# Kernel optimization log

Measured on AMD Instinct MI355X. Metric: run time of the kernel, lower is better.

The kernel has to match this reference:

```python
import jax, jax.numpy as jnp
import numpy as np
import math

B, R, C = 4, 512, 512
E, H, D, M, F = 256, 16, 16, 16, 512  # embed, heads, qkv_dim, ms_hidden, ff_hidden
EPS = 1e-5


def setup_inputs() -> dict:
    key = jax.random.key(0)
    ks = jax.random.split(key, 20)
    s = lambda fan_in: 1.0 / math.sqrt(fan_in)
    u = lambda k, shape, lim: jax.random.uniform(k, shape, jnp.float32, -lim, lim)
    mix1_init = (1 / 2) ** 0.5
    mix2_init = (1 / 16) ** 0.5
    return {
        "row_emb": jax.random.normal(ks[0], (B, R, E), jnp.float32),
        "col_emb": jax.random.normal(ks[1], (B, C, E), jnp.float32),
        "cost_mat": jax.random.uniform(ks[2], (B, R, C), jnp.float32),
        "Wq": u(ks[3], (E, H * D), s(E)),
        "Wk": u(ks[4], (E, H * D), s(E)),
        "Wv": u(ks[5], (E, H * D), s(E)),
        "mix1_w": u(ks[6], (H, 2, M), mix1_init),
        "mix1_b": u(ks[7], (H, M), mix1_init),
        "mix2_w": u(ks[8], (H, M, 1), mix2_init),
        "mix2_b": u(ks[9], (H, 1), mix2_init),
        "Wc": u(ks[10], (H * D, E), s(H * D)),
        "bc": u(ks[11], (E,), s(H * D)),
        "W1": u(ks[12], (E, F), s(E)),
        "b1": u(ks[13], (F,), s(E)),
        "W2": u(ks[14], (F, E), s(F)),
        "b2": u(ks[15], (E,), s(F)),
        "g1": jnp.ones((E,), jnp.float32),
        "be1": jnp.zeros((E,), jnp.float32),
        "g2": jnp.ones((E,), jnp.float32),
        "be2": jnp.zeros((E,), jnp.float32),
    }


def _instance_norm(x, gamma, beta):
    # InstanceNorm1d on x permuted to (B, E, L): normalize over seq dim per (b, channel)
    mean = jnp.mean(x, axis=1, keepdims=True)          # [B,1,E]
    var = jnp.mean((x - mean) ** 2, axis=1, keepdims=True)
    return (x - mean) * jax.lax.rsqrt(var + EPS) * gamma + beta


def reference(row_emb, col_emb, cost_mat, Wq, Wk, Wv, mix1_w, mix1_b, mix2_w,
              mix2_b, Wc, bc, W1, b1, W2, b2, g1, be1, g2, be2):
    # QKV projections, split heads: [B,L,H*D] -> [B,H,L,D]
    q = (row_emb @ Wq).reshape(B, R, H, D).transpose(0, 2, 1, 3)
    k = (col_emb @ Wk).reshape(B, C, H, D).transpose(0, 2, 1, 3)
    v = (col_emb @ Wv).reshape(B, C, H, D).transpose(0, 2, 1, 3)

    dot = jnp.einsum('bhrd,bhcd->bhrc', q, k) / math.sqrt(D)
    cost = jnp.broadcast_to(cost_mat[:, None, :, :], (B, H, R, C))
    two = jnp.stack((dot, cost), axis=-1)               # [B,H,R,C,2]

    # per-head 2 -> M -> 1 mixing MLP over scores
    ms1 = jnp.einsum('bhrcs,hsm->bhrcm', two, mix1_w) + mix1_b[None, :, None, None, :]
    ms1 = jax.nn.relu(ms1)
    mixed = jnp.einsum('bhrcm,hm->bhrc', ms1, mix2_w[:, :, 0]) + mix2_b[:, 0][None, :, None, None]

    weights = jax.nn.softmax(mixed, axis=-1)            # [B,H,R,C]
    out = jnp.einsum('bhrc,bhcd->bhrd', weights, v)
    out_concat = out.transpose(0, 2, 1, 3).reshape(B, R, H * D)

    mh = out_concat @ Wc + bc                           # multi_head_combine

    # TransformerFFN with instance norm
    x = _instance_norm(row_emb + mh, g1, be1)
    ffn = jax.nn.relu(x @ W1 + b1) @ W2 + b2
    return _instance_norm(x + ffn, g2, be2)
```

## Files before the change

### kernel.cpp

```cpp
#include <hip/hip_runtime.h>
#include <hip/hip_bf16.h>

typedef __hip_bfloat16 bf16;
typedef __hip_bfloat162 bf162;
typedef _Float16 f16;
typedef __attribute__((ext_vector_type(2))) _Float16 h2;
typedef __attribute__((ext_vector_type(8))) short short8;
typedef __attribute__((ext_vector_type(4))) float f32x4;

#define B_ 4
#define R_ 512
#define C_ 512
#define E_ 256
#define H_ 16
#define D_ 16

__device__ __forceinline__ float b2f(bf16 x) { return __bfloat162float(x); }
__device__ __forceinline__ void stout(bf16* p, float v) { *p = __float2bfloat16(v); }
__device__ __forceinline__ void stout(f16* p, float v) { *p = (f16)v; }

__device__ __forceinline__ float fdot2(h2 a, h2 b, float c) {
#if __has_builtin(__builtin_amdgcn_fdot2)
    return __builtin_amdgcn_fdot2(a, b, c, false);
#else
    return (float)a.x * (float)b.x + (float)a.y * (float)b.y + c;
#endif
}

__global__ __launch_bounds__(256) void transpose_cvt_kernel(
    const float* __restrict__ Wq, const float* __restrict__ Wk, const float* __restrict__ Wv,
    const float* __restrict__ Wc, const float* __restrict__ W1, const float* __restrict__ W2,
    bf16* __restrict__ WqT, bf16* __restrict__ WkT, bf16* __restrict__ WvT,
    bf16* __restrict__ WcT, bf16* __restrict__ W1T, bf16* __restrict__ W2T,
    float* __restrict__ statsZ)
{
    __shared__ bf16 tile[32][33];
    const int wsel = blockIdx.y;
    const int tx = blockIdx.x;
    if (wsel == 0 && tx >= 64) {
        const int idx = (tx - 64) * 256 + threadIdx.x;
        if (idx < 4096) statsZ[idx] = 0.f;
        return;
    }
    const float* src; bf16* dst; int K, N;
    switch (wsel) {
        case 0: src = Wq; dst = WqT; K = 256; N = 256; break;
        case 1: src = Wk; dst = WkT; K = 256; N = 256; break;
        case 2: src = Wv; dst = WvT; K = 256; N = 256; break;
        case 3: src = Wc; dst = WcT; K = 256; N = 256; break;
        case 4: src = W1; dst = W1T; K = 256; N = 512; break;
        default: src = W2; dst = W2T; K = 512; N = 256; break;
    }
    const int ntiles = (K >> 5) * (N >> 5);
    if (tx >= ntiles) return;
    const int ncnt = N >> 5;
    const int tk = tx / ncnt, tn = tx % ncnt;
    const int c = threadIdx.x & 31, r = threadIdx.x >> 5;
#pragma unroll
    for (int i = 0; i < 4; i++)
        tile[r + i * 8][c] = __float2bfloat16(src[(size_t)(tk * 32 + r + i * 8) * N + tn * 32 + c]);
    __syncthreads();
#pragma unroll
    for (int i = 0; i < 4; i++)
        dst[(size_t)(tn * 32 + r + i * 8) * K + tk * 32 + c] = tile[c][r + i * 8];
}

template <int AMODE, typename OT, int BM, int BN, bool BIAS, int RES, bool RELU, bool STATS>
__device__ __forceinline__ void mfma_gemm_body(
    const void* __restrict__ Ap, const bf16* __restrict__ plA,
    const bf16* __restrict__ BT, const float* __restrict__ bias,
    const void* __restrict__ Res,
    const float* __restrict__ normS, const float* __restrict__ normG, const float* __restrict__ normB,
    float* __restrict__ statsOut, OT* __restrict__ Cout,
    int M, int N, int K, int bx, int by)
{
    constexpr int MT = BM / 32, NT = BN / 32;
    constexpr int AEL = BM * 64 / 256, BEL = BN * 64 / 256;
    __shared__ __align__(16) bf16 As[BM * 80];
    __shared__ __align__(16) bf16 Bs[BN * 80];
    const int tid = threadIdx.x;
    const int wid = tid >> 6, lane = tid & 63;
    const int wm = wid >> 1, wn = wid & 1;
    const int fr = lane & 15, quad = lane >> 4;
    const int m0 = by * BM, n0 = bx * BN;
    const int arow = (AEL == 16) ? (tid >> 2) : (tid >> 3);
    const int akg  = (AEL == 16) ? ((tid & 3) << 4) : ((tid & 7) << 3);
    const int brow = (BEL == 16) ? (tid >> 2) : (tid >> 3);
    const int bkg  = (BEL == 16) ? ((tid & 3) << 4) : ((tid & 7) << 3);

    f32x4 acc[MT][NT];
#pragma unroll
    for (int mt = 0; mt < MT; mt++)
#pragma unroll
        for (int nt = 0; nt < NT; nt++) acc[mt][nt] = (f32x4){0.f, 0.f, 0.f, 0.f};

    for (int k0 = 0; k0 < K; k0 += 64) {
        if constexpr (AMODE == 0) {
            const short8* gp = (const short8*)((const bf16*)Ap + (size_t)(m0 + arow) * K + k0 + akg);
#pragma unroll
            for (int t8 = 0; t8 < AEL / 8; t8++) *(short8*)(&As[arow * 80 + akg + 8 * t8]) = gp[t8];
        } else if constexpr (AMODE == 1) {
            const float4* gp = (const float4*)((const float*)Ap + (size_t)(m0 + arow) * K + k0 + akg);
#pragma unroll
            for (int j = 0; j < AEL / 4; j++) {
                const float4 f = gp[j];
                *(bf162*)(&As[arow * 80 + akg + j * 4])     = __float22bfloat162_rn(make_float2(f.x, f.y));
                *(bf162*)(&As[arow * 80 + akg + j * 4 + 2]) = __float22bfloat162_rn(make_float2(f.z, f.w));
            }
        } else if constexpr (AMODE == 2) {
            const int bb = (m0 + arow) >> 9;
            const bf16* ap = (const bf16*)Ap + (size_t)(m0 + arow) * K + k0 + akg;
            bf16 tmp[AEL];
#pragma unroll
            for (int t8 = 0; t8 < AEL / 8; t8++) *(short8*)(tmp + 8 * t8) = ((const short8*)ap)[t8];
#pragma unroll
            for (int j = 0; j < AEL; j++) {
                const int e = k0 + akg + j;
                const float s = normS[bb * 256 + e], sq = normS[1024 + bb * 256 + e];
                const float mn = s * (1.f / 512.f);
                float var = sq * (1.f / 512.f) - mn * mn; var = fmaxf(var, 0.f);
                As[arow * 80 + akg + j] = __float2bfloat16(
                    (b2f(tmp[j]) - mn) * rsqrtf(var + 1e-5f) * normG[e] + normB[e]);
            }
        } else {
            const int row = m0 + arow;
            const int bb = row >> 9, rr2 = row & 511;
            const int e0 = k0 + akg;
            const int hh = e0 >> 4, d0 = e0 & 15;
            const int idx = ((bb * 16 + hh) << 9) + rr2;
            const float l0 = b2f(plA[idx]), l1 = b2f(plA[32768 + idx]);
            const float l2 = b2f(plA[65536 + idx]), l3 = b2f(plA[98304 + idx]);
            const float inv = 1.f / (l0 + l1 + l2 + l3);
            const bf16* pob = (const bf16*)Ap;
            float a8[8] = {};
#pragma unroll
            for (int c = 0; c < 4; c++) {
                const float wgt = ((c == 0) ? l0 : (c == 1) ? l1 : (c == 2) ? l2 : l3) * inv;
                const bf162* pp = (const bf162*)(pob + (size_t)(c * 32768 + idx) * 16 + d0);
#pragma unroll
                for (int j = 0; j < 4; j++) {
                    const float2 f = __bfloat1622float2(pp[j]);
                    a8[2 * j]     = fmaf(wgt, f.x, a8[2 * j]);
                    a8[2 * j + 1] = fmaf(wgt, f.y, a8[2 * j + 1]);
                }
            }
#pragma unroll
            for (int j = 0; j < 8; j++)
                As[arow * 80 + akg + j] = __float2bfloat16(a8[j]);
        }
        {
            const short8* gp = (const short8*)(BT + (size_t)(n0 + brow) * K + k0 + bkg);
#pragma unroll
            for (int t8 = 0; t8 < BEL / 8; t8++) *(short8*)(&Bs[brow * 80 + bkg + 8 * t8]) = gp[t8];
        }
        __syncthreads();

        short8 af[MT][2], bfr[NT][2];
#pragma unroll
        for (int mt = 0; mt < MT; mt++) {
            const int ar = wm * (BM / 2) + mt * 16 + fr;
#pragma unroll
            for (int kh = 0; kh < 2; kh++)
                af[mt][kh] = *(const short8*)(&As[ar * 80 + quad * 8 + kh * 32]);
        }
#pragma unroll
        for (int nt = 0; nt < NT; nt++) {
            const int br = wn * (BN / 2) + nt * 16 + fr;
#pragma unroll
            for (int kh = 0; kh < 2; kh++)
                bfr[nt][kh] = *(const short8*)(&Bs[br * 80 + quad * 8 + kh * 32]);
        }
#pragma unroll
        for (int kh = 0; kh < 2; kh++)
#pragma unroll
            for (int mt = 0; mt < MT; mt++)
#pragma unroll
                for (int nt = 0; nt < NT; nt++)
                    acc[mt][nt] = __builtin_amdgcn_mfma_f32_16x16x32_bf16(
                        af[mt][kh], bfr[nt][kh], acc[mt][nt], 0, 0, 0);
        __syncthreads();
    }

    float vsum[NT], vss[NT];
#pragma unroll
    for (int nt = 0; nt < NT; nt++) { vsum[nt] = 0.f; vss[nt] = 0.f; }
#pragma unroll
    for (int mt = 0; mt < MT; mt++) {
#pragma unroll
        for (int nt = 0; nt < NT; nt++) {
#pragma unroll
            for (int i = 0; i < 4; i++) {
                const int row = m0 + wm * (BM / 2) + mt * 16 + quad * 4 + i;
                const int col = n0 + wn * (BN / 2) + nt * 16 + fr;
                float v = acc[mt][nt][i];
                if (BIAS) v += bias[col];
                if constexpr (RES == 1) v += ((const float*)Res)[(size_t)row * N + col];
                if constexpr (RES == 3) {
                    const int bb = row >> 9;
                    const float yv = b2f(((const bf16*)Res)[(size_t)row * N + col]);
                    const float s = normS[bb * 256 + col], sq = normS[1024 + bb * 256 + col];
                    const float mn = s * (1.f / 512.f);
                    float var = sq * (1.f / 512.f) - mn * mn; var = fmaxf(var, 0.f);
                    v += (yv - mn) * rsqrtf(var + 1e-5f) * normG[col] + normB[col];
                }
                if (RELU) v = fmaxf(v, 0.f);
                stout(&Cout[(size_t)row * N + col], v);
                if (STATS) { vsum[nt] += v; vss[nt] += v * v; }
            }
        }
    }
    if constexpr (STATS) {
        float* sred = (float*)As;
#pragma unroll
        for (int nt = 0; nt < NT; nt++) {
            float a = vsum[nt]; a += __shfl_xor(a, 16, 64); a += __shfl_xor(a, 32, 64);
            float c = vss[nt];  c += __shfl_xor(c, 16, 64); c += __shfl_xor(c, 32, 64);
            if (quad == 0) {
                const int cl = wn * (BN / 2) + nt * 16 + fr;
                sred[wm * (2 * BN) + cl * 2 + 0] = a;
                sred[wm * (2 * BN) + cl * 2 + 1] = c;
            }
        }
        __syncthreads();
        if (tid < 2 * BN) {
            const int cl = tid >> 1, w = tid & 1;
            const float tot = sred[cl * 2 + w] + sred[2 * BN + cl * 2 + w];
            atomicAdd(&statsOut[w * 1024 + (m0 >> 9) * 256 + n0 + cl], tot);
        }
    }
}

template <int AMODE, typename OT, int BM, int BN, bool BIAS, int RES, bool RELU, bool STATS>
__global__ __launch_bounds__(256) void mfma_gemm_kernel(
    const void* __restrict__ Ap, const bf16* __restrict__ plA,
    const bf16* __restrict__ BT, const float* __restrict__ bias,
    const void* __restrict__ Res,
    const float* __restrict__ normS, const float* __restrict__ normG, const float* __restrict__ normB,
    float* __restrict__ statsOut, OT* __restrict__ Cout, int M, int N, int K)
{
    mfma_gemm_body<AMODE, OT, BM, BN, BIAS, RES, RELU, STATS>(
        Ap, plA, BT, bias, Res, normS, normG, normB, statsOut, Cout,
        M, N, K, blockIdx.x, blockIdx.y);
}

__global__ __launch_bounds__(256) void qkv_kernel(
    const float* __restrict__ rowE, const float* __restrict__ colE,
    const bf16* __restrict__ WqT, const bf16* __restrict__ WkT, const bf16* __restrict__ WvT,
    f16* __restrict__ qo, f16* __restrict__ ko, f16* __restrict__ vo)
{
    const int z = blockIdx.z;
    const float* A = (z == 0) ? rowE : colE;
    const bf16* BT = (z == 0) ? WqT : (z == 1) ? WkT : WvT;
    f16* O = (z == 0) ? qo : (z == 1) ? ko : vo;
    mfma_gemm_body<1, f16, 32, 64, false, 0, false, false>(
        A, nullptr, BT, nullptr, nullptr, nullptr, nullptr, nullptr, nullptr, O,
        2048, 256, 256, blockIdx.x, blockIdx.y);
}

__global__ __launch_bounds__(256) void attn_kernel(
    const f16* __restrict__ q, const f16* __restrict__ k, const f16* __restrict__ v,
    const float* __restrict__ cost, const float* __restrict__ m1w, const float* __restrict__ m1b,
    const float* __restrict__ m2w, const float* __restrict__ m2b,
    bf16* __restrict__ po, bf16* __restrict__ plb)
{
    __shared__ __align__(16) char slds[17408];
    f16* kbuf = (f16*)slds;
    float* vbuf = (float*)(slds + 4096);
    float* sm = (float*)slds;

    const int rt = blockIdx.x >> 2, cs = blockIdx.x & 3;
    const int h = blockIdx.y, b = blockIdx.z;
    const int tid = threadIdx.x, wid = tid >> 6, lane = tid & 63;

    {
        const size_t base = ((size_t)b * C_) * 256 + h * 16 + (size_t)cs * 128 * 256;
        const int lc = tid >> 1, dp = (tid & 1) * 8;
        const size_t g = base + (size_t)lc * 256 + dp;
        *(short8*)(&kbuf[lc * 16 + dp]) = *(const short8*)(k + g);
        const short8 vraw = *(const short8*)(v + g);
        const h2* rh = (const h2*)&vraw;
        *(float4*)(&vbuf[lc * 16 + dp]) = make_float4(
            (float)rh[0].x, (float)rh[0].y, (float)rh[1].x, (float)rh[1].y);
        *(float4*)(&vbuf[lc * 16 + dp + 4]) = make_float4(
            (float)rh[2].x, (float)rh[2].y, (float)rh[3].x, (float)rh[3].y);
    }

    h2 w1a2[8], w1b2[8], b1h[8], w2p[8];
#pragma unroll
    for (int i = 0; i < 8; i++) {
        h2 t;
        t.x = (f16)m1w[h * 32 + 2 * i];      t.y = (f16)m1w[h * 32 + 2 * i + 1];      w1a2[i] = t;
        t.x = (f16)m1w[h * 32 + 16 + 2 * i]; t.y = (f16)m1w[h * 32 + 17 + 2 * i];     w1b2[i] = t;
        t.x = (f16)m1b[h * 16 + 2 * i];      t.y = (f16)m1b[h * 16 + 2 * i + 1];      b1h[i] = t;
        t.x = (f16)m2w[h * 16 + 2 * i];      t.y = (f16)m2w[h * 16 + 2 * i + 1];      w2p[i] = t;
    }
    const float b2v = m2b[h];
    const h2 zero2 = (h2)(f16)0;

    const int r = rt * 64 + lane;
    short8 qraw[2];
    {
        const short8* qp = (const short8*)(q + (size_t)(b * R_ + r) * 256 + h * 16);
        qraw[0] = qp[0]; qraw[1] = qp[1];
    }
    const h2* qh = (const h2*)qraw;

    __syncthreads();

    const float* crow = cost + (size_t)(b * R_ + r) * C_ + cs * 128 + wid * 32;
    float lrun = 0.f;
    float o[16] = {};

    for (int cc = 0; cc < 32; cc += 4) {
        const float4 cst4 = *(const float4*)(crow + cc);
#pragma unroll
        for (int u = 0; u < 4; u++) {
            const int lc = wid * 32 + cc + u;
            const h2* kr = (const h2*)(&kbuf[lc * 16]);
            float d = 0.f;
#pragma unroll
            for (int i = 0; i < 8; i++) d = fdot2(qh[i], kr[i], d);
            const float dot = d * 0.25f;
            const float cst = (u == 0) ? cst4.x : (u == 1) ? cst4.y : (u == 2) ? cst4.z : cst4.w;
            const f16 doth = (f16)dot, csth = (f16)cst;
            h2 dot2; dot2.x = doth; dot2.y = doth;
            h2 cst2; cst2.x = csth; cst2.y = csth;
            float acc = b2v;
#pragma unroll
            for (int i = 0; i < 8; i++) {
                h2 t = dot2 * w1a2[i] + b1h[i];
                t = cst2 * w1b2[i] + t;
                t = __builtin_elementwise_max(t, zero2);
                acc = fdot2(t, w2p[i], acc);
            }
            const float p = __expf(acc);
            lrun += p;
            const float4* vr = (const float4*)(&vbuf[lc * 16]);
            const float4 v0 = vr[0], v1 = vr[1], v2 = vr[2], v3 = vr[3];
            o[0]  = fmaf(p, v0.x, o[0]);  o[1]  = fmaf(p, v0.y, o[1]);
            o[2]  = fmaf(p, v0.z, o[2]);  o[3]  = fmaf(p, v0.w, o[3]);
            o[4]  = fmaf(p, v1.x, o[4]);  o[5]  = fmaf(p, v1.y, o[5]);
            o[6]  = fmaf(p, v1.z, o[6]);  o[7]  = fmaf(p, v1.w, o[7]);
            o[8]  = fmaf(p, v2.x, o[8]);  o[9]  = fmaf(p, v2.y, o[9]);
            o[10] = fmaf(p, v2.z, o[10]); o[11] = fmaf(p, v2.w, o[11]);
            o[12] = fmaf(p, v3.x, o[12]); o[13] = fmaf(p, v3.y, o[13]);
            o[14] = fmaf(p, v3.z, o[14]); o[15] = fmaf(p, v3.w, o[15]);
        }
    }

    __syncthreads();
    sm[wid * 64 + lane] = lrun;
    {
        float* p = &sm[256 + (wid * 64 + lane) * 16];
#pragma unroll
        for (int d = 0; d < 16; d++) p[d] = o[d];
    }
    __syncthreads();

    if (tid < 64) {
        const int rr = tid;
        float ll = 0.f, oo[16] = {};
#pragma unroll
        for (int w = 0; w < 4; w++) {
            ll += sm[w * 64 + rr];
            const float* p = &sm[256 + (w * 64 + rr) * 16];
#pragma unroll
            for (int d = 0; d < 16; d++) oo[d] += p[d];
        }
        const float inv = 1.f / ll;
        const int idx = ((b * H_ + h) << 9) + rt * 64 + rr;
        plb[cs * 32768 + idx] = __float2bfloat16(ll);
        bf162* pp = (bf162*)(po + (size_t)(cs * 32768 + idx) * 16);
#pragma unroll
        for (int j = 0; j < 8; j++)
            pp[j] = __float22bfloat162_rn(make_float2(oo[2 * j] * inv, oo[2 * j + 1] * inv));
    }
}

__global__ __launch_bounds__(256) void apply_in2_kernel(
    const bf16* __restrict__ xin, const float* __restrict__ stats,
    const float* __restrict__ g, const float* __restrict__ be, float* __restrict__ outp)
{
    const int base = (blockIdx.x * 256 + threadIdx.x) * 4;
    const int b = base >> 17;
    const bf162* xp = (const bf162*)(xin + base);
    const float2 x0 = __bfloat1622float2(xp[0]), x1 = __bfloat1622float2(xp[1]);
    const float xv[4] = {x0.x, x0.y, x1.x, x1.y};
    float4 rr;
    float* rp = (float*)&rr;
#pragma unroll
    for (int j = 0; j < 4; j++) {
        const int e = (base & 255) + j;
        const float s = stats[b * 256 + e], sq = stats[1024 + b * 256 + e];
        const float mn = s * (1.f / 512.f);
        float var = sq * (1.f / 512.f) - mn * mn; var = fmaxf(var, 0.f);
        rp[j] = (xv[j] - mn) * rsqrtf(var + 1e-5f) * g[e] + be[e];
    }
    *(float4*)(outp + base) = rr;
}

extern "C" void kernel_launch(void* const* d_in, const int* in_sizes, int n_in,
                              void* d_out, int out_size, void* d_ws, size_t ws_size,
                              hipStream_t stream)
{
    (void)in_sizes; (void)n_in; (void)out_size; (void)ws_size;
    const float* row_emb = (const float*)d_in[0];
    const float* col_emb = (const float*)d_in[1];
    const float* cost    = (const float*)d_in[2];
    const float* Wq  = (const float*)d_in[3];
    const float* Wk  = (const float*)d_in[4];
    const float* Wv  = (const float*)d_in[5];
    const float* m1w = (const float*)d_in[6];
    const float* m1b = (const float*)d_in[7];
    const float* m2w = (const float*)d_in[8];
    const float* m2b = (const float*)d_in[9];
    const float* Wc  = (const float*)d_in[10];
    const float* bc  = (const float*)d_in[11];
    const float* W1  = (const float*)d_in[12];
    const float* b1  = (const float*)d_in[13];
    const float* W2  = (const float*)d_in[14];
    const float* b2  = (const float*)d_in[15];
    const float* g1  = (const float*)d_in[16];
    const float* be1 = (const float*)d_in[17];
    const float* g2  = (const float*)d_in[18];
    const float* be2 = (const float*)d_in[19];
    float* out = (float*)d_out;

    char* w = (char*)d_ws;
    f16*  sq  = (f16*)(w + 0);
    f16*  sk  = (f16*)(w + 1048576);
    f16*  sv  = (f16*)(w + 2097152);
    bf16* sy  = (bf16*)(w + 0);
    bf16* shm = (bf16*)(w + 1048576);
    bf16* WqT = (bf16*)(w + 3145728);
    bf16* WkT = WqT + 65536;
    bf16* WvT = WkT + 65536;
    bf16* po  = (bf16*)(w + 3145728);
    bf16* st  = (bf16*)(w + 3145728);
    bf16* plb = (bf16*)(w + 7340032);
    bf16* WcT = (bf16*)(w + 7602176);
    bf16* W1T = (bf16*)(w + 7733248);
    bf16* W2T = (bf16*)(w + 7995392);
    float* stats1 = (float*)(w + 8257536);
    float* stats2 = stats1 + 2048;

    const dim3 blk(256);

    transpose_cvt_kernel<<<dim3(128, 6), blk, 0, stream>>>(
        Wq, Wk, Wv, Wc, W1, W2, WqT, WkT, WvT, WcT, W1T, W2T, stats1);

    qkv_kernel<<<dim3(4, 64, 3), blk, 0, stream>>>(row_emb, col_emb, WqT, WkT, WvT, sq, sk, sv);

    attn_kernel<<<dim3(32, 16, 4), blk, 0, stream>>>(
        sq, sk, sv, cost, m1w, m1b, m2w, m2b, po, plb);

    mfma_gemm_kernel<3, bf16, 32, 32, true, 1, false, true><<<dim3(8, 64), blk, 0, stream>>>(
        po, plb, WcT, bc, row_emb, nullptr, nullptr, nullptr, stats1, sy, 2048, 256, 256);

    mfma_gemm_kernel<2, bf16, 32, 64, true, 0, true, false><<<dim3(8, 64), blk, 0, stream>>>(
        sy, nullptr, W1T, b1, nullptr, stats1, g1, be1, nullptr, shm, 2048, 512, 256);

    mfma_gemm_kernel<0, bf16, 32, 32, true, 3, false, true><<<dim3(8, 64), blk, 0, stream>>>(
        shm, nullptr, W2T, b2, sy, stats1, g1, be1, stats2, st, 2048, 256, 512);

    apply_in2_kernel<<<dim3(512), blk, 0, stream>>>(st, stats2, g2, be2, out);
}
```

Before: 168.7 us.

## Split attention partial merge into its own kernel and pack PV accumulation

Moves the merge of the four column-split attention partials out of the Wc GEMM's A-tile loader into a separate attn_merge_kernel that writes a dense bf16 activation, so the GEMM uses the plain bf16 load path. It also rewrites the P·V accumulation in the attention kernel using two-wide float vectors, which may let the compiler emit packed FMA. Workspace buffers are reassigned to fit the new intermediate. This adds an extra kernel launch and a round trip of the merged activation through global memory.

```diff
diff --git a/kernel.cpp b/kernel.cpp
--- a/kernel.cpp
+++ b/kernel.cpp
@@ -7,6 +7,7 @@
 typedef __attribute__((ext_vector_type(2))) _Float16 h2;
 typedef __attribute__((ext_vector_type(8))) short short8;
 typedef __attribute__((ext_vector_type(4))) float f32x4;
+typedef __attribute__((ext_vector_type(2))) float f32x2;
 
 #define B_ 4
 #define R_ 512
@@ -67,7 +68,7 @@
 
 template <int AMODE, typename OT, int BM, int BN, bool BIAS, int RES, bool RELU, bool STATS>
 __device__ __forceinline__ void mfma_gemm_body(
-    const void* __restrict__ Ap, const bf16* __restrict__ plA,
+    const void* __restrict__ Ap,
     const bf16* __restrict__ BT, const float* __restrict__ bias,
     const void* __restrict__ Res,
     const float* __restrict__ normS, const float* __restrict__ normG, const float* __restrict__ normB,
@@ -107,7 +108,7 @@
                 *(bf162*)(&As[arow * 80 + akg + j * 4])     = __float22bfloat162_rn(make_float2(f.x, f.y));
                 *(bf162*)(&As[arow * 80 + akg + j * 4 + 2]) = __float22bfloat162_rn(make_float2(f.z, f.w));
             }
-        } else if constexpr (AMODE == 2) {
+        } else {
             const int bb = (m0 + arow) >> 9;
             const bf16* ap = (const bf16*)Ap + (size_t)(m0 + arow) * K + k0 + akg;
             bf16 tmp[AEL];
@@ -122,31 +123,6 @@
                 As[arow * 80 + akg + j] = __float2bfloat16(
                     (b2f(tmp[j]) - mn) * rsqrtf(var + 1e-5f) * normG[e] + normB[e]);
             }
-        } else {
-            const int row = m0 + arow;
-            const int bb = row >> 9, rr2 = row & 511;
-            const int e0 = k0 + akg;
-            const int hh = e0 >> 4, d0 = e0 & 15;
-            const int idx = ((bb * 16 + hh) << 9) + rr2;
-            const float l0 = b2f(plA[idx]), l1 = b2f(plA[32768 + idx]);
-            const float l2 = b2f(plA[65536 + idx]), l3 = b2f(plA[98304 + idx]);
-            const float inv = 1.f / (l0 + l1 + l2 + l3);
-            const bf16* pob = (const bf16*)Ap;
-            float a8[8] = {};
-#pragma unroll
-            for (int c = 0; c < 4; c++) {
-                const float wgt = ((c == 0) ? l0 : (c == 1) ? l1 : (c == 2) ? l2 : l3) * inv;
-                const bf162* pp = (const bf162*)(pob + (size_t)(c * 32768 + idx) * 16 + d0);
-#pragma unroll
-                for (int j = 0; j < 4; j++) {
-                    const float2 f = __bfloat1622float2(pp[j]);
-                    a8[2 * j]     = fmaf(wgt, f.x, a8[2 * j]);
-                    a8[2 * j + 1] = fmaf(wgt, f.y, a8[2 * j + 1]);
-                }
-            }
-#pragma unroll
-            for (int j = 0; j < 8; j++)
-                As[arow * 80 + akg + j] = __float2bfloat16(a8[j]);
         }
         {
             const short8* gp = (const short8*)(BT + (size_t)(n0 + brow) * K + k0 + bkg);
@@ -232,14 +208,14 @@
 
 template <int AMODE, typename OT, int BM, int BN, bool BIAS, int RES, bool RELU, bool STATS>
 __global__ __launch_bounds__(256) void mfma_gemm_kernel(
-    const void* __restrict__ Ap, const bf16* __restrict__ plA,
+    const void* __restrict__ Ap,
     const bf16* __restrict__ BT, const float* __restrict__ bias,
     const void* __restrict__ Res,
     const float* __restrict__ normS, const float* __restrict__ normG, const float* __restrict__ normB,
     float* __restrict__ statsOut, OT* __restrict__ Cout, int M, int N, int K)
 {
     mfma_gemm_body<AMODE, OT, BM, BN, BIAS, RES, RELU, STATS>(
-        Ap, plA, BT, bias, Res, normS, normG, normB, statsOut, Cout,
+        Ap, BT, bias, Res, normS, normG, normB, statsOut, Cout,
         M, N, K, blockIdx.x, blockIdx.y);
 }
 
@@ -253,7 +229,7 @@
     const bf16* BT = (z == 0) ? WqT : (z == 1) ? WkT : WvT;
     f16* O = (z == 0) ? qo : (z == 1) ? ko : vo;
     mfma_gemm_body<1, f16, 32, 64, false, 0, false, false>(
-        A, nullptr, BT, nullptr, nullptr, nullptr, nullptr, nullptr, nullptr, O,
+        A, BT, nullptr, nullptr, nullptr, nullptr, nullptr, nullptr, O,
         2048, 256, 256, blockIdx.x, blockIdx.y);
 }
 
@@ -309,7 +285,9 @@
 
     const float* crow = cost + (size_t)(b * R_ + r) * C_ + cs * 128 + wid * 32;
     float lrun = 0.f;
-    float o[16] = {};
+    f32x2 o2[8];
+#pragma unroll
+    for (int j = 0; j < 8; j++) o2[j] = (f32x2){0.f, 0.f};
 
     for (int cc = 0; cc < 32; cc += 4) {
         const float4 cst4 = *(const float4*)(crow + cc);
@@ -335,16 +313,10 @@
             }
             const float p = __expf(acc);
             lrun += p;
-            const float4* vr = (const float4*)(&vbuf[lc * 16]);
-            const float4 v0 = vr[0], v1 = vr[1], v2 = vr[2], v3 = vr[3];
-            o[0]  = fmaf(p, v0.x, o[0]);  o[1]  = fmaf(p, v0.y, o[1]);
-            o[2]  = fmaf(p, v0.z, o[2]);  o[3]  = fmaf(p, v0.w, o[3]);
-            o[4]  = fmaf(p, v1.x, o[4]);  o[5]  = fmaf(p, v1.y, o[5]);
-            o[6]  = fmaf(p, v1.z, o[6]);  o[7]  = fmaf(p, v1.w, o[7]);
-            o[8]  = fmaf(p, v2.x, o[8]);  o[9]  = fmaf(p, v2.y, o[9]);
-            o[10] = fmaf(p, v2.z, o[10]); o[11] = fmaf(p, v2.w, o[11]);
-            o[12] = fmaf(p, v3.x, o[12]); o[13] = fmaf(p, v3.y, o[13]);
-            o[14] = fmaf(p, v3.z, o[14]); o[15] = fmaf(p, v3.w, o[15]);
+            f32x2 p2; p2.x = p; p2.y = p;
+            const f32x2* vr = (const f32x2*)(&vbuf[lc * 16]);
+#pragma unroll
+            for (int j = 0; j < 8; j++) o2[j] = p2 * vr[j] + o2[j];
         }
     }
 
@@ -353,7 +325,7 @@
     {
         float* p = &sm[256 + (wid * 64 + lane) * 16];
 #pragma unroll
-        for (int d = 0; d < 16; d++) p[d] = o[d];
+        for (int j = 0; j < 8; j++) { p[2 * j] = o2[j].x; p[2 * j + 1] = o2[j].y; }
     }
     __syncthreads();
 
@@ -375,6 +347,32 @@
         for (int j = 0; j < 8; j++)
             pp[j] = __float22bfloat162_rn(make_float2(oo[2 * j] * inv, oo[2 * j + 1] * inv));
     }
+}
+
+__global__ __launch_bounds__(256) void attn_merge_kernel(
+    const bf16* __restrict__ po, const bf16* __restrict__ plb, bf16* __restrict__ sa)
+{
+    const int idx = blockIdx.x * 256 + threadIdx.x;
+    const float l0 = b2f(plb[idx]), l1 = b2f(plb[32768 + idx]);
+    const float l2 = b2f(plb[65536 + idx]), l3 = b2f(plb[98304 + idx]);
+    const float inv = 1.f / (l0 + l1 + l2 + l3);
+    float oo[16] = {};
+#pragma unroll
+    for (int c = 0; c < 4; c++) {
+        const float wgt = ((c == 0) ? l0 : (c == 1) ? l1 : (c == 2) ? l2 : l3) * inv;
+        const bf162* pp = (const bf162*)(po + (size_t)(c * 32768 + idx) * 16);
+#pragma unroll
+        for (int j = 0; j < 8; j++) {
+            const float2 f = __bfloat1622float2(pp[j]);
+            oo[2 * j]     = fmaf(wgt, f.x, oo[2 * j]);
+            oo[2 * j + 1] = fmaf(wgt, f.y, oo[2 * j + 1]);
+        }
+    }
+    const int b = idx >> 13, h = (idx >> 9) & 15, r = idx & 511;
+    bf162* dst = (bf162*)(sa + (size_t)(b * R_ + r) * 256 + h * 16);
+#pragma unroll
+    for (int j = 0; j < 8; j++)
+        dst[j] = __float22bfloat162_rn(make_float2(oo[2 * j], oo[2 * j + 1]));
 }
 
 __global__ __launch_bounds__(256) void apply_in2_kernel(
@@ -430,13 +428,14 @@
     f16*  sq  = (f16*)(w + 0);
     f16*  sk  = (f16*)(w + 1048576);
     f16*  sv  = (f16*)(w + 2097152);
-    bf16* sy  = (bf16*)(w + 0);
-    bf16* shm = (bf16*)(w + 1048576);
+    bf16* sa  = (bf16*)(w + 0);
+    bf16* sy  = (bf16*)(w + 1048576);
+    bf16* st  = (bf16*)(w + 2097152);
     bf16* WqT = (bf16*)(w + 3145728);
     bf16* WkT = WqT + 65536;
     bf16* WvT = WkT + 65536;
     bf16* po  = (bf16*)(w + 3145728);
-    bf16* st  = (bf16*)(w + 3145728);
+    bf16* shm = (bf16*)(w + 3145728);
     bf16* plb = (bf16*)(w + 7340032);
     bf16* WcT = (bf16*)(w + 7602176);
     bf16* W1T = (bf16*)(w + 7733248);
@@ -454,14 +453,16 @@
     attn_kernel<<<dim3(32, 16, 4), blk, 0, stream>>>(
         sq, sk, sv, cost, m1w, m1b, m2w, m2b, po, plb);
 
-    mfma_gemm_kernel<3, bf16, 32, 32, true, 1, false, true><<<dim3(8, 64), blk, 0, stream>>>(
-        po, plb, WcT, bc, row_emb, nullptr, nullptr, nullptr, stats1, sy, 2048, 256, 256);
+    attn_merge_kernel<<<dim3(128), blk, 0, stream>>>(po, plb, sa);
+
+    mfma_gemm_kernel<0, bf16, 32, 32, true, 1, false, true><<<dim3(8, 64), blk, 0, stream>>>(
+        sa, WcT, bc, row_emb, nullptr, nullptr, nullptr, stats1, sy, 2048, 256, 256);
 
     mfma_gemm_kernel<2, bf16, 32, 64, true, 0, true, false><<<dim3(8, 64), blk, 0, stream>>>(
-        sy, nullptr, W1T, b1, nullptr, stats1, g1, be1, nullptr, shm, 2048, 512, 256);
+        sy, W1T, b1, nullptr, stats1, g1, be1, nullptr, shm, 2048, 512, 256);
 
     mfma_gemm_kernel<0, bf16, 32, 32, true, 3, false, true><<<dim3(8, 64), blk, 0, stream>>>(
-        shm, nullptr, W2T, b2, sy, stats1, g1, be1, stats2, st, 2048, 256, 512);
+        shm, W2T, b2, sy, stats1, g1, be1, stats2, st, 2048, 256, 512);
 
     apply_in2_kernel<<<dim3(512), blk, 0, stream>>>(st, stats2, g2, be2, out);
 }
```

Measured after the change: 165.8 us. No clear change (-1.7%).
